# Kernel optimization log

Hardware: AMD Instinct MI355X
Metric: run time of the kernel (lower is better)

The kernel has to match this reference:

```python
import jax, jax.numpy as jnp
import numpy as np

# config (mirrors scaled-down DeepSeekModelConfig)
B, S, H = 2, 512, 1024          # batch, seq, hidden_size
E, I = 64, 512                  # n_routed_experts, moe_intermediate_size
K = 8                           # num_experts_per_tok
G, TG = 8, 4                    # n_group, topk_group
SCALE = 2.5                     # routed_scaling_factor
T = B * S                       # tokens
CAP = 512


def setup_inputs() -> dict:
    key = jax.random.key(0)
    ks = jax.random.split(key, 9)
    s_h = 1.0 / np.sqrt(H)
    s_i = 1.0 / np.sqrt(I)
    return {
        "x": jax.random.normal(ks[0], (B, S, H), jnp.float32),
        "router_w": jax.random.normal(ks[1], (H, E), jnp.float32) * s_h,
        "gate_w": jax.random.normal(ks[2], (E, H, I), jnp.float32) * s_h,
        "up_w": jax.random.normal(ks[3], (E, H, I), jnp.float32) * s_h,
        "down_w": jax.random.normal(ks[4], (E, I, H), jnp.float32) * s_i,
        "shared_gate_w": jax.random.normal(ks[5], (H, I), jnp.float32) * s_h,
        "shared_up_w": jax.random.normal(ks[6], (H, I), jnp.float32) * s_h,
        "shared_down_w": jax.random.normal(ks[7], (I, H), jnp.float32) * s_i,
    }


def _moe_forward(x, router_w, gate_w, up_w, down_w, shared_gate_w, shared_up_w, shared_down_w):
    b, s, h = x.shape
    tokens = x.reshape(-1, h)                              # [T, H]
    t = tokens.shape[0]

    # ---- router: sigmoid scores + grouped top-k masking ----
    logits = tokens @ router_w                             # [T, E]
    scores = jax.nn.sigmoid(logits)
    eg = E // G
    group_scores = scores.reshape(t, G, eg).max(axis=-1)   # [T, G]
    _, sel_groups = jax.lax.top_k(group_scores, TG)        # [T, TG]
    group_mask = jnp.zeros((t, G), bool).at[jnp.arange(t)[:, None], sel_groups].set(True)
    expert_mask = jnp.repeat(group_mask, eg, axis=1)       # [T, E]
    masked_scores = jnp.where(expert_mask, scores, 0.0)

    topk_w, topk_idx = jax.lax.top_k(masked_scores, K)     # [T, K]
    topk_w = topk_w / jnp.clip(topk_w.sum(-1, keepdims=True), 1e-9)
    topk_w = topk_w * SCALE

    # ---- dispatch: scatter tokens into per-expert capacity buffers ----
    flat_e = topk_idx.reshape(-1)                          # [T*K] expert id per assignment (row-major t,k)
    onehot = jax.nn.one_hot(flat_e, E, dtype=jnp.int32)    # [T*K, E]
    prior = jnp.cumsum(onehot, axis=0) - onehot            # exclusive count per expert
    pos = jnp.take_along_axis(prior, flat_e[:, None], axis=1)[:, 0]  # slot within expert
    valid = (pos < CAP).astype(tokens.dtype)               # [T*K]
    pos_c = jnp.minimum(pos, CAP - 1)
    tidx = jnp.repeat(jnp.arange(t), K)                    # token id per assignment

    dispatch = jnp.zeros((E, CAP, h), tokens.dtype)
    dispatch = dispatch.at[flat_e, pos_c].add(tokens[tidx] * valid[:, None])  # [E, C, H]

    # ---- per-expert SwiGLU (grouped GEMM) ----
    g = jnp.einsum('ech,ehi->eci', dispatch, gate_w)
    u = jnp.einsum('ech,ehi->eci', dispatch, up_w)
    expert_out = jnp.einsum('eci,eih->ech', jax.nn.silu(g) * u, down_w)       # [E, C, H]

    # ---- combine: gather back and weighted scatter-add ----
    gathered = expert_out[flat_e, pos_c]                   # [T*K, H]
    contrib = gathered * (topk_w.reshape(-1) * valid)[:, None]
    output = jnp.zeros((t, h), tokens.dtype).at[tidx].add(contrib)

    # ---- shared expert (n_shared_experts = 1) ----
    sg = jax.nn.silu(tokens @ shared_gate_w) * (tokens @ shared_up_w)
    output = output + sg @ shared_down_w
    return output.reshape(b, s, h)


def reference(x, router_w, gate_w, up_w, down_w, shared_gate_w, shared_up_w, shared_down_w):
    return _moe_forward(x, router_w, gate_w, up_w, down_w,
                        shared_gate_w, shared_up_w, shared_down_w)
```

## Files before the change

### kernel.cpp

```cpp
#include <hip/hip_runtime.h>
#include <hip/hip_bf16.h>

#define T_TOK 1024
#define H_DIM 1024
#define E_NUM 64
#define I_DIM 512
#define K_TOP 8
#define TG_NUM 4
#define CAPC 512
#define RSCALE 2.5f

typedef __attribute__((ext_vector_type(8))) short bf16x8;
typedef __attribute__((ext_vector_type(4))) float f32x4;

__device__ __forceinline__ ushort f2bf(float f) {
    union { float f; unsigned u; } v; v.f = f;
    unsigned r = v.u + 0x7fffu + ((v.u >> 16) & 1u);
    return (ushort)(r >> 16);
}
__device__ __forceinline__ unsigned pk2(float lo, float hi) {
    return (unsigned)f2bf(lo) | ((unsigned)f2bf(hi) << 16);
}
__device__ __forceinline__ void ldsbar() {
    asm volatile("s_waitcnt lgkmcnt(0)" ::: "memory");
    __builtin_amdgcn_s_barrier();
}

__global__ __launch_bounds__(256) void k_router(
    const float* __restrict__ x, const float* __restrict__ rw,
    ushort* __restrict__ xb,
    int* __restrict__ cnt, int* __restrict__ exp_tok,
    int* __restrict__ tslot, float* __restrict__ tw)
{
    const int t    = blockIdx.x;
    const int lane = threadIdx.x & 63;
    const int w    = threadIdx.x >> 6;

    {
        const float4 v = *(const float4*)&x[(size_t)t * H_DIM + threadIdx.x * 4];
        ushort4 o; o.x = f2bf(v.x); o.y = f2bf(v.y); o.z = f2bf(v.z); o.w = f2bf(v.w);
        *(ushort4*)&xb[(size_t)t * H_DIM + threadIdx.x * 4] = o;
    }

    const float* xp = x + (size_t)t * H_DIM + w * 256;
    const float* wp = rw + (size_t)(w * 256) * E_NUM + lane;
    float acc = 0.f;
    #pragma unroll 8
    for (int i = 0; i < 256; ++i)
        acc += xp[i] * wp[(size_t)i * E_NUM];

    __shared__ float part[4][64];
    part[w][lane] = acc;
    __syncthreads();
    if (threadIdx.x >= 64) return;

    float logit = part[0][lane] + part[1][lane] + part[2][lane] + part[3][lane];
    float score = 1.f / (1.f + expf(-logit));

    float gm = score;
    gm = fmaxf(gm, __shfl_xor(gm, 1));
    gm = fmaxf(gm, __shfl_xor(gm, 2));
    gm = fmaxf(gm, __shfl_xor(gm, 4));
    const int myg = lane >> 3;
    int grank = 0;
    #pragma unroll
    for (int j = 0; j < 8; ++j) {
        float gj = __shfl(gm, j * 8);
        grank += (gj > gm) || (gj == gm && j < myg);
    }
    float masked = (grank < TG_NUM) ? score : 0.f;

    int erank = 0;
    for (int j = 0; j < 64; ++j) {
        float sj = __shfl(masked, j);
        erank += (sj > masked) || (sj == masked && j < lane);
    }
    const bool keep = (erank < K_TOP);

    float kv = keep ? masked : 0.f;
    kv += __shfl_xor(kv, 1);  kv += __shfl_xor(kv, 2);  kv += __shfl_xor(kv, 4);
    kv += __shfl_xor(kv, 8);  kv += __shfl_xor(kv, 16); kv += __shfl_xor(kv, 32);
    const float wgt = masked / fmaxf(kv, 1e-9f) * RSCALE;

    if (keep) {
        int slot = atomicAdd(&cnt[lane], 1);
        if (slot < CAPC) {
            exp_tok[lane * CAPC + slot] = t;
            tslot[t * K_TOP + erank] = (lane << 9) | slot;
            tw[t * K_TOP + erank]    = wgt;
        } else {
            tslot[t * K_TOP + erank] = (lane << 9);
            tw[t * K_TOP + erank]    = 0.f;
        }
    }
}

__global__ void k_scan(const int* __restrict__ cnt, int* __restrict__ offs)
{
    const int lane = threadIdx.x;
    int v = min(cnt[lane], CAPC);
    #pragma unroll
    for (int off = 1; off < 64; off <<= 1) {
        int u = __shfl_up(v, off);
        if (lane >= off) v += u;
    }
    offs[lane + 1] = v;
    if (lane == 0) offs[0] = 0;
}

__global__ __launch_bounds__(512) void k_gemm1(
    const ushort* __restrict__ xb,
    const float* __restrict__ gate_w, const float* __restrict__ up_w,
    const float* __restrict__ sgate_w, const float* __restrict__ sup_w,
    const int* __restrict__ cnt, const int* __restrict__ offs,
    const int* __restrict__ exp_tok,
    ushort* __restrict__ hbuf)
{
    const int mt = blockIdx.x, nb = blockIdx.y, e = blockIdx.z;
    const bool sh = (e >= E_NUM);
    const int m0 = mt * 128;
    const int Me = sh ? 128 : min(cnt[e], CAPC);
    if (m0 >= Me) return;
    const int Mt = min(128, Me - m0);
    const int obase = sh ? (offs[E_NUM] + (e - E_NUM) * 128) : (offs[e] + m0);
    const float* gw = sh ? sgate_w : gate_w + (size_t)e * (H_DIM * I_DIM);
    const float* uw = sh ? sup_w  : up_w  + (size_t)e * (H_DIM * I_DIM);
    const int n0 = nb * 64;

    __shared__ ushort Bls[2 * 2 * 4096];

    const int tid  = threadIdx.x;
    const int lane = tid & 63, wid = tid >> 6;
    const int wm = wid >> 1, wn = wid & 1;
    const int fr = lane & 15, fg = lane >> 4;

    const int r0 = wm * 32 + fr, r1 = r0 + 16;
    int t0, t1;
    if (sh) { t0 = (e - E_NUM) * 128 + r0; t1 = (e - E_NUM) * 128 + r1; }
    else {
        t0 = (r0 < Mt) ? exp_tok[e * CAPC + m0 + r0] : 0;
        t1 = (r1 < Mt) ? exp_tok[e * CAPC + m0 + r1] : 0;
    }
    const ushort* a0p = xb + (size_t)t0 * H_DIM + fg * 8;
    const ushort* a1p = xb + (size_t)t1 * H_DIM + fg * 8;

    const int kp = tid >> 4, q = tid & 15;
    const float* gp = gw + (size_t)(2 * kp) * I_DIM + n0 + q * 4;
    const float* up = uw + (size_t)(2 * kp) * I_DIM + n0 + q * 4;
    const int wbe = (kp >> 2) * 512 + (kp & 3) * 2 + q * 32;

    f32x4 accg[2][2], accu[2][2];
    #pragma unroll
    for (int a = 0; a < 2; ++a)
        #pragma unroll
        for (int b = 0; b < 2; ++b) { accg[a][b] = (f32x4)0.f; accu[a][b] = (f32x4)0.f; }

    float4 pg0 = *(const float4*)gp;
    float4 pg1 = *(const float4*)(gp + I_DIM);
    float4 pu0 = *(const float4*)up;
    float4 pu1 = *(const float4*)(up + I_DIM);

    const int NT = H_DIM / 64;
    for (int kt = 0; kt < NT; ++kt) {
        float4 g0 = pg0, g1 = pg1, u0 = pu0, u1 = pu1;
        ushort* bw = &Bls[(kt & 1) * 8192 + wbe];
        #pragma unroll
        for (int j = 0; j < 4; ++j) {
            *(unsigned*)&bw[j * 8]        = pk2(((const float*)&g0)[j], ((const float*)&g1)[j]);
            *(unsigned*)&bw[4096 + j * 8] = pk2(((const float*)&u0)[j], ((const float*)&u1)[j]);
        }
        ldsbar();

        bf16x8 a00 = *(const bf16x8*)&a0p[kt * 64];
        bf16x8 a01 = *(const bf16x8*)&a0p[kt * 64 + 32];
        bf16x8 a10 = *(const bf16x8*)&a1p[kt * 64];
        bf16x8 a11 = *(const bf16x8*)&a1p[kt * 64 + 32];

        if (kt < NT - 1) {
            const float* gn = gp + (size_t)(kt + 1) * 64 * I_DIM;
            const float* un = up + (size_t)(kt + 1) * 64 * I_DIM;
            pg0 = *(const float4*)gn;  pg1 = *(const float4*)(gn + I_DIM);
            pu0 = *(const float4*)un;  pu1 = *(const float4*)(un + I_DIM);
        }

        const ushort* br = &Bls[(kt & 1) * 8192 + fg * 512 + (wn * 32 + fr) * 8];
        #pragma unroll
        for (int ks = 0; ks < 2; ++ks) {
            bf16x8 bg0 = *(const bf16x8*)&br[ks * 2048];
            bf16x8 bg1 = *(const bf16x8*)&br[ks * 2048 + 128];
            bf16x8 bu0 = *(const bf16x8*)&br[4096 + ks * 2048];
            bf16x8 bu1 = *(const bf16x8*)&br[4096 + ks * 2048 + 128];
            bf16x8 aa0 = ks ? a01 : a00;
            bf16x8 aa1 = ks ? a11 : a10;
            accg[0][0] = __builtin_amdgcn_mfma_f32_16x16x32_bf16(aa0, bg0, accg[0][0], 0, 0, 0);
            accg[0][1] = __builtin_amdgcn_mfma_f32_16x16x32_bf16(aa0, bg1, accg[0][1], 0, 0, 0);
            accg[1][0] = __builtin_amdgcn_mfma_f32_16x16x32_bf16(aa1, bg0, accg[1][0], 0, 0, 0);
            accg[1][1] = __builtin_amdgcn_mfma_f32_16x16x32_bf16(aa1, bg1, accg[1][1], 0, 0, 0);
            accu[0][0] = __builtin_amdgcn_mfma_f32_16x16x32_bf16(aa0, bu0, accu[0][0], 0, 0, 0);
            accu[0][1] = __builtin_amdgcn_mfma_f32_16x16x32_bf16(aa0, bu1, accu[0][1], 0, 0, 0);
            accu[1][0] = __builtin_amdgcn_mfma_f32_16x16x32_bf16(aa1, bu0, accu[1][0], 0, 0, 0);
            accu[1][1] = __builtin_amdgcn_mfma_f32_16x16x32_bf16(aa1, bu1, accu[1][1], 0, 0, 0);
        }
    }

    #pragma unroll
    for (int fm = 0; fm < 2; ++fm)
        #pragma unroll
        for (int fn = 0; fn < 2; ++fn)
            #pragma unroll
            for (int r = 0; r < 4; ++r) {
                const int l = wm * 32 + fm * 16 + fg * 4 + r;
                if (l < Mt) {
                    float g = accg[fm][fn][r];
                    float u = accu[fm][fn][r];
                    float h = g / (1.f + expf(-g)) * u;
                    hbuf[(size_t)(obase + l) * I_DIM + n0 + wn * 32 + fn * 16 + fr] = f2bf(h);
                }
            }
}

__global__ __launch_bounds__(512) void k_gemm2(
    const ushort* __restrict__ hbuf,
    const float* __restrict__ down_w, const float* __restrict__ sdown_w,
    const int* __restrict__ cnt, const int* __restrict__ offs,
    float* __restrict__ obuf)
{
    const int mt = blockIdx.x, nb = blockIdx.y, e = blockIdx.z;
    const bool sh = (e >= E_NUM);
    const int m0 = mt * 128;
    const int Me = sh ? 128 : min(cnt[e], CAPC);
    if (m0 >= Me) return;
    const int Mt = min(128, Me - m0);
    const int obase = sh ? (offs[E_NUM] + (e - E_NUM) * 128) : (offs[e] + m0);
    const float* dw = sh ? sdown_w : down_w + (size_t)e * (I_DIM * H_DIM);
    const int n0 = nb * 64;

    __shared__ ushort Bls[2 * 4096];

    const int tid  = threadIdx.x;
    const int lane = tid & 63, wid = tid >> 6;
    const int wm = wid >> 1, wn = wid & 1;
    const int fr = lane & 15, fg = lane >> 4;

    const ushort* a0p = hbuf + (size_t)(obase + wm * 32 + fr) * I_DIM + fg * 8;
    const ushort* a1p = a0p + (size_t)16 * I_DIM;

    const int kp = tid >> 4, q = tid & 15;
    const float* gp = dw + (size_t)(2 * kp) * H_DIM + n0 + q * 4;
    const int wbe = (kp >> 2) * 512 + (kp & 3) * 2 + q * 32;

    f32x4 acc[2][2];
    #pragma unroll
    for (int a = 0; a < 2; ++a)
        #pragma unroll
        for (int b = 0; b < 2; ++b) acc[a][b] = (f32x4)0.f;

    float4 pg0 = *(const float4*)gp;
    float4 pg1 = *(const float4*)(gp + H_DIM);

    const int NT = I_DIM / 64;
    for (int kt = 0; kt < NT; ++kt) {
        float4 g0 = pg0, g1 = pg1;
        ushort* bw = &Bls[(kt & 1) * 4096 + wbe];
        #pragma unroll
        for (int j = 0; j < 4; ++j)
            *(unsigned*)&bw[j * 8] = pk2(((const float*)&g0)[j], ((const float*)&g1)[j]);
        ldsbar();

        bf16x8 a00 = *(const bf16x8*)&a0p[kt * 64];
        bf16x8 a01 = *(const bf16x8*)&a0p[kt * 64 + 32];
        bf16x8 a10 = *(const bf16x8*)&a1p[kt * 64];
        bf16x8 a11 = *(const bf16x8*)&a1p[kt * 64 + 32];

        if (kt < NT - 1) {
            const float* gn = gp + (size_t)(kt + 1) * 64 * H_DIM;
            pg0 = *(const float4*)gn;  pg1 = *(const float4*)(gn + H_DIM);
        }

        const ushort* br = &Bls[(kt & 1) * 4096 + fg * 512 + (wn * 32 + fr) * 8];
        #pragma unroll
        for (int ks = 0; ks < 2; ++ks) {
            bf16x8 b0 = *(const bf16x8*)&br[ks * 2048];
            bf16x8 b1 = *(const bf16x8*)&br[ks * 2048 + 128];
            bf16x8 aa0 = ks ? a01 : a00;
            bf16x8 aa1 = ks ? a11 : a10;
            acc[0][0] = __builtin_amdgcn_mfma_f32_16x16x32_bf16(aa0, b0, acc[0][0], 0, 0, 0);
            acc[0][1] = __builtin_amdgcn_mfma_f32_16x16x32_bf16(aa0, b1, acc[0][1], 0, 0, 0);
            acc[1][0] = __builtin_amdgcn_mfma_f32_16x16x32_bf16(aa1, b0, acc[1][0], 0, 0, 0);
            acc[1][1] = __builtin_amdgcn_mfma_f32_16x16x32_bf16(aa1, b1, acc[1][1], 0, 0, 0);
        }
    }

    #pragma unroll
    for (int fm = 0; fm < 2; ++fm)
        #pragma unroll
        for (int fn = 0; fn < 2; ++fn)
            #pragma unroll
            for (int r = 0; r < 4; ++r) {
                const int l = wm * 32 + fm * 16 + fg * 4 + r;
                if (l < Mt)
                    obuf[(size_t)(obase + l) * H_DIM + n0 + wn * 32 + fn * 16 + fr] = acc[fm][fn][r];
            }
}

__global__ __launch_bounds__(256) void k_combine(
    const float* __restrict__ obuf, const int* __restrict__ offs,
    const int* __restrict__ tslot, const float* __restrict__ tw,
    float* __restrict__ out)
{
    const int t = blockIdx.x;
    __shared__ int   rs[8];
    __shared__ float wss[8];
    if (threadIdx.x < 8) {
        int id = tslot[t * K_TOP + threadIdx.x];
        rs[threadIdx.x]  = offs[id >> 9] + (id & 511);
        wss[threadIdx.x] = tw[t * K_TOP + threadIdx.x];
    }
    __syncthreads();
    const int c = threadIdx.x * 4;
    const int shrow = offs[E_NUM] + t;
    float4 acc = *(const float4*)&obuf[(size_t)shrow * H_DIM + c];
    #pragma unroll
    for (int j = 0; j < 8; ++j) {
        float4 v = *(const float4*)&obuf[(size_t)rs[j] * H_DIM + c];
        float w = wss[j];
        acc.x += w * v.x; acc.y += w * v.y; acc.z += w * v.z; acc.w += w * v.w;
    }
    *(float4*)&out[(size_t)t * H_DIM + c] = acc;
}

extern "C" void kernel_launch(void* const* d_in, const int* in_sizes, int n_in,
                              void* d_out, int out_size, void* d_ws, size_t ws_size,
                              hipStream_t stream)
{
    const float* x       = (const float*)d_in[0];
    const float* rw      = (const float*)d_in[1];
    const float* gate_w  = (const float*)d_in[2];
    const float* up_w    = (const float*)d_in[3];
    const float* down_w  = (const float*)d_in[4];
    const float* sgate_w = (const float*)d_in[5];
    const float* sup_w   = (const float*)d_in[6];
    const float* sdown_w = (const float*)d_in[7];
    float* out = (float*)d_out;

    char* ws = (char*)d_ws;
    int*    cnt     = (int*)(ws + 0);
    int*    offs    = (int*)(ws + 256);
    int*    exp_tok = (int*)(ws + 1024);
    int*    tslot   = (int*)(ws + 1024 + 131072);
    float*  tw      = (float*)(ws + 1024 + 131072 + 32768);
    ushort* xb      = (ushort*)(ws + (512u << 10));
    ushort* hbuf    = (ushort*)(ws + (3u << 20));
    float*  obuf    = (float*)(ws + (13u << 20));

    hipMemsetAsync(cnt, 0, 256, stream);
    k_router<<<T_TOK, 256, 0, stream>>>(x, rw, xb, cnt, exp_tok, tslot, tw);
    k_scan<<<1, 64, 0, stream>>>(cnt, offs);
    k_gemm1<<<dim3(2, 8, 72), 512, 0, stream>>>(xb, gate_w, up_w, sgate_w, sup_w,
                                                cnt, offs, exp_tok, hbuf);
    k_gemm2<<<dim3(2, 16, 72), 512, 0, stream>>>(hbuf, down_w, sdown_w, cnt, offs, obuf);
    k_combine<<<T_TOK, 256, 0, stream>>>(obuf, offs, tslot, tw, out);
}
```

Measured before the change: 542.7 us.

## Deepen weight/activation prefetch and use coalesced scalar weight loads in expert GEMMs

Both expert GEMM kernels now prefetch fp32 weights two K-tiles ahead and activation fragments one tile ahead in register double buffers, with the K loop fully unrolled. Weight loads change from per-thread float4 to strided scalar loads (q, q+16, ...), so adjacent lanes read adjacent addresses, and the LDS write pattern is remapped to match. Launch bounds now request 4 blocks per CU. The aim is to hide global-load latency behind MFMA work, at the cost of more registers and more load instructions, and the occupancy hint may force register spills.

```diff
diff --git a/kernel.cpp b/kernel.cpp
--- a/kernel.cpp
+++ b/kernel.cpp
@@ -108,7 +108,7 @@
     if (lane == 0) offs[0] = 0;
 }
 
-__global__ __launch_bounds__(512) void k_gemm1(
+__global__ __launch_bounds__(512, 4) void k_gemm1(
     const ushort* __restrict__ xb,
     const float* __restrict__ gate_w, const float* __restrict__ up_w,
     const float* __restrict__ sgate_w, const float* __restrict__ sup_w,
@@ -127,7 +127,7 @@
     const float* uw = sh ? sup_w  : up_w  + (size_t)e * (H_DIM * I_DIM);
     const int n0 = nb * 64;
 
-    __shared__ ushort Bls[2 * 2 * 4096];
+    __shared__ ushort Bls[2 * 8192];
 
     const int tid  = threadIdx.x;
     const int lane = tid & 63, wid = tid >> 6;
@@ -145,9 +145,10 @@
     const ushort* a1p = xb + (size_t)t1 * H_DIM + fg * 8;
 
     const int kp = tid >> 4, q = tid & 15;
-    const float* gp = gw + (size_t)(2 * kp) * I_DIM + n0 + q * 4;
-    const float* up = uw + (size_t)(2 * kp) * I_DIM + n0 + q * 4;
-    const int wbe = (kp >> 2) * 512 + (kp & 3) * 2 + q * 32;
+    const int kc = kp >> 2, c = kp & 3;
+    const float* gp  = gw + (size_t)(2 * kp) * I_DIM + n0 + q;
+    const float* upp = uw + (size_t)(2 * kp) * I_DIM + n0 + q;
+    const int wbase = kc * 512 + q * 8 + c * 2;
 
     f32x4 accg[2][2], accu[2][2];
     #pragma unroll
@@ -155,43 +156,46 @@
         #pragma unroll
         for (int b = 0; b < 2; ++b) { accg[a][b] = (f32x4)0.f; accu[a][b] = (f32x4)0.f; }
 
-    float4 pg0 = *(const float4*)gp;
-    float4 pg1 = *(const float4*)(gp + I_DIM);
-    float4 pu0 = *(const float4*)up;
-    float4 pu1 = *(const float4*)(up + I_DIM);
-
-    const int NT = H_DIM / 64;
-    for (int kt = 0; kt < NT; ++kt) {
-        float4 g0 = pg0, g1 = pg1, u0 = pu0, u1 = pu1;
-        ushort* bw = &Bls[(kt & 1) * 8192 + wbe];
+    float wg0[2][4], wg1[2][4], wu0[2][4], wu1[2][4];
+    bf16x8 av[2][4];
+
+#define LOADW1(p, kt) {                                                        \
+    const float* g_ = gp  + (size_t)(kt) * 64 * I_DIM;                         \
+    const float* u_ = upp + (size_t)(kt) * 64 * I_DIM;                         \
+    wg0[p][0]=g_[0];  wg0[p][1]=g_[16]; wg0[p][2]=g_[32]; wg0[p][3]=g_[48];    \
+    wg1[p][0]=g_[I_DIM]; wg1[p][1]=g_[I_DIM+16]; wg1[p][2]=g_[I_DIM+32]; wg1[p][3]=g_[I_DIM+48]; \
+    wu0[p][0]=u_[0];  wu0[p][1]=u_[16]; wu0[p][2]=u_[32]; wu0[p][3]=u_[48];    \
+    wu1[p][0]=u_[I_DIM]; wu1[p][1]=u_[I_DIM+16]; wu1[p][2]=u_[I_DIM+32]; wu1[p][3]=u_[I_DIM+48]; }
+#define LOADA1(p, kt) {                                                        \
+    av[p][0] = *(const bf16x8*)&a0p[(kt) * 64];                                \
+    av[p][1] = *(const bf16x8*)&a0p[(kt) * 64 + 32];                           \
+    av[p][2] = *(const bf16x8*)&a1p[(kt) * 64];                                \
+    av[p][3] = *(const bf16x8*)&a1p[(kt) * 64 + 32]; }
+
+    LOADW1(0, 0); LOADA1(0, 0); LOADW1(1, 1);
+
+    #pragma unroll
+    for (int kt = 0; kt < 16; ++kt) {
+        const int p = kt & 1;
+        ushort* bw = &Bls[p * 8192 + wbase];
         #pragma unroll
         for (int j = 0; j < 4; ++j) {
-            *(unsigned*)&bw[j * 8]        = pk2(((const float*)&g0)[j], ((const float*)&g1)[j]);
-            *(unsigned*)&bw[4096 + j * 8] = pk2(((const float*)&u0)[j], ((const float*)&u1)[j]);
+            *(unsigned*)&bw[j * 128]        = pk2(wg0[p][j], wg1[p][j]);
+            *(unsigned*)&bw[4096 + j * 128] = pk2(wu0[p][j], wu1[p][j]);
         }
         ldsbar();
-
-        bf16x8 a00 = *(const bf16x8*)&a0p[kt * 64];
-        bf16x8 a01 = *(const bf16x8*)&a0p[kt * 64 + 32];
-        bf16x8 a10 = *(const bf16x8*)&a1p[kt * 64];
-        bf16x8 a11 = *(const bf16x8*)&a1p[kt * 64 + 32];
-
-        if (kt < NT - 1) {
-            const float* gn = gp + (size_t)(kt + 1) * 64 * I_DIM;
-            const float* un = up + (size_t)(kt + 1) * 64 * I_DIM;
-            pg0 = *(const float4*)gn;  pg1 = *(const float4*)(gn + I_DIM);
-            pu0 = *(const float4*)un;  pu1 = *(const float4*)(un + I_DIM);
-        }
-
-        const ushort* br = &Bls[(kt & 1) * 8192 + fg * 512 + (wn * 32 + fr) * 8];
+        if (kt + 2 < 16) LOADW1(p, kt + 2);
+        if (kt + 1 < 16) LOADA1(1 - p, kt + 1);
+
+        const ushort* br = &Bls[p * 8192 + fg * 512 + (wn * 32 + fr) * 8];
         #pragma unroll
         for (int ks = 0; ks < 2; ++ks) {
             bf16x8 bg0 = *(const bf16x8*)&br[ks * 2048];
             bf16x8 bg1 = *(const bf16x8*)&br[ks * 2048 + 128];
             bf16x8 bu0 = *(const bf16x8*)&br[4096 + ks * 2048];
             bf16x8 bu1 = *(const bf16x8*)&br[4096 + ks * 2048 + 128];
-            bf16x8 aa0 = ks ? a01 : a00;
-            bf16x8 aa1 = ks ? a11 : a10;
+            bf16x8 aa0 = ks ? av[p][1] : av[p][0];
+            bf16x8 aa1 = ks ? av[p][3] : av[p][2];
             accg[0][0] = __builtin_amdgcn_mfma_f32_16x16x32_bf16(aa0, bg0, accg[0][0], 0, 0, 0);
             accg[0][1] = __builtin_amdgcn_mfma_f32_16x16x32_bf16(aa0, bg1, accg[0][1], 0, 0, 0);
             accg[1][0] = __builtin_amdgcn_mfma_f32_16x16x32_bf16(aa1, bg0, accg[1][0], 0, 0, 0);
@@ -202,6 +206,8 @@
             accu[1][1] = __builtin_amdgcn_mfma_f32_16x16x32_bf16(aa1, bu1, accu[1][1], 0, 0, 0);
         }
     }
+#undef LOADW1
+#undef LOADA1
 
     #pragma unroll
     for (int fm = 0; fm < 2; ++fm)
@@ -219,7 +225,7 @@
             }
 }
 
-__global__ __launch_bounds__(512) void k_gemm2(
+__global__ __launch_bounds__(512, 4) void k_gemm2(
     const ushort* __restrict__ hbuf,
     const float* __restrict__ down_w, const float* __restrict__ sdown_w,
     const int* __restrict__ cnt, const int* __restrict__ offs,
@@ -246,8 +252,9 @@
     const ushort* a1p = a0p + (size_t)16 * I_DIM;
 
     const int kp = tid >> 4, q = tid & 15;
-    const float* gp = dw + (size_t)(2 * kp) * H_DIM + n0 + q * 4;
-    const int wbe = (kp >> 2) * 512 + (kp & 3) * 2 + q * 32;
+    const int kc = kp >> 2, c = kp & 3;
+    const float* dp = dw + (size_t)(2 * kp) * H_DIM + n0 + q;
+    const int wbase = kc * 512 + q * 8 + c * 2;
 
     f32x4 acc[2][2];
     #pragma unroll
@@ -255,41 +262,47 @@
         #pragma unroll
         for (int b = 0; b < 2; ++b) acc[a][b] = (f32x4)0.f;
 
-    float4 pg0 = *(const float4*)gp;
-    float4 pg1 = *(const float4*)(gp + H_DIM);
-
-    const int NT = I_DIM / 64;
-    for (int kt = 0; kt < NT; ++kt) {
-        float4 g0 = pg0, g1 = pg1;
-        ushort* bw = &Bls[(kt & 1) * 4096 + wbe];
+    float wd0[2][4], wd1[2][4];
+    bf16x8 av[2][4];
+
+#define LOADW2(p, kt) {                                                        \
+    const float* d_ = dp + (size_t)(kt) * 64 * H_DIM;                          \
+    wd0[p][0]=d_[0];  wd0[p][1]=d_[16]; wd0[p][2]=d_[32]; wd0[p][3]=d_[48];    \
+    wd1[p][0]=d_[H_DIM]; wd1[p][1]=d_[H_DIM+16]; wd1[p][2]=d_[H_DIM+32]; wd1[p][3]=d_[H_DIM+48]; }
+#define LOADA2(p, kt) {                                                        \
+    av[p][0] = *(const bf16x8*)&a0p[(kt) * 64];                                \
+    av[p][1] = *(const bf16x8*)&a0p[(kt) * 64 + 32];                           \
+    av[p][2] = *(const bf16x8*)&a1p[(kt) * 64];                                \
+    av[p][3] = *(const bf16x8*)&a1p[(kt) * 64 + 32]; }
+
+    LOADW2(0, 0); LOADA2(0, 0); LOADW2(1, 1);
+
+    #pragma unroll
+    for (int kt = 0; kt < 8; ++kt) {
+        const int p = kt & 1;
+        ushort* bw = &Bls[p * 4096 + wbase];
         #pragma unroll
         for (int j = 0; j < 4; ++j)
-            *(unsigned*)&bw[j * 8] = pk2(((const float*)&g0)[j], ((const float*)&g1)[j]);
+            *(unsigned*)&bw[j * 128] = pk2(wd0[p][j], wd1[p][j]);
         ldsbar();
-
-        bf16x8 a00 = *(const bf16x8*)&a0p[kt * 64];
-        bf16x8 a01 = *(const bf16x8*)&a0p[kt * 64 + 32];
-        bf16x8 a10 = *(const bf16x8*)&a1p[kt * 64];
-        bf16x8 a11 = *(const bf16x8*)&a1p[kt * 64 + 32];
-
-        if (kt < NT - 1) {
-            const float* gn = gp + (size_t)(kt + 1) * 64 * H_DIM;
-            pg0 = *(const float4*)gn;  pg1 = *(const float4*)(gn + H_DIM);
-        }
-
-        const ushort* br = &Bls[(kt & 1) * 4096 + fg * 512 + (wn * 32 + fr) * 8];
+        if (kt + 2 < 8) LOADW2(p, kt + 2);
+        if (kt + 1 < 8) LOADA2(1 - p, kt + 1);
+
+        const ushort* br = &Bls[p * 4096 + fg * 512 + (wn * 32 + fr) * 8];
         #pragma unroll
         for (int ks = 0; ks < 2; ++ks) {
             bf16x8 b0 = *(const bf16x8*)&br[ks * 2048];
             bf16x8 b1 = *(const bf16x8*)&br[ks * 2048 + 128];
-            bf16x8 aa0 = ks ? a01 : a00;
-            bf16x8 aa1 = ks ? a11 : a10;
+            bf16x8 aa0 = ks ? av[p][1] : av[p][0];
+            bf16x8 aa1 = ks ? av[p][3] : av[p][2];
             acc[0][0] = __builtin_amdgcn_mfma_f32_16x16x32_bf16(aa0, b0, acc[0][0], 0, 0, 0);
             acc[0][1] = __builtin_amdgcn_mfma_f32_16x16x32_bf16(aa0, b1, acc[0][1], 0, 0, 0);
             acc[1][0] = __builtin_amdgcn_mfma_f32_16x16x32_bf16(aa1, b0, acc[1][0], 0, 0, 0);
             acc[1][1] = __builtin_amdgcn_mfma_f32_16x16x32_bf16(aa1, b1, acc[1][1], 0, 0, 0);
         }
     }
+#undef LOADW2
+#undef LOADA2
 
     #pragma unroll
     for (int fm = 0; fm < 2; ++fm)
```

Measured after the change: 541.5 us. About the same (-0.2%).

## Loop over M tiles per block and deepen weight prefetch pipeline in expert GEMMs

Applied to the files above, without the earlier changes.

Each block in both grouped GEMMs now walks every 128-row M tile of its expert instead of launching a separate block per M tile. The grid drops a dimension and blocks whose tile would be empty are no longer launched. The K loop is restructured into an even/odd double-buffered pipeline with a K-step of 32, a smaller LDS footprint, float2 weight loads, and a launch-bounds occupancy hint of 4. Blocks handling experts with more than 128 tokens re-read and re-convert the fp32 weights for each tile. Heavily loaded experts are also serialised within one block, which may hurt load balance.

```diff
diff --git a/kernel.cpp b/kernel.cpp
--- a/kernel.cpp
+++ b/kernel.cpp
@@ -12,6 +12,8 @@
 
 typedef __attribute__((ext_vector_type(8))) short bf16x8;
 typedef __attribute__((ext_vector_type(4))) float f32x4;
+
+#define MFMA_BF16 __builtin_amdgcn_mfma_f32_16x16x32_bf16
 
 __device__ __forceinline__ ushort f2bf(float f) {
     union { float f; unsigned u; } v; v.f = f;
@@ -108,7 +110,7 @@
     if (lane == 0) offs[0] = 0;
 }
 
-__global__ __launch_bounds__(512) void k_gemm1(
+__global__ __launch_bounds__(512, 4) void k_gemm1(
     const ushort* __restrict__ xb,
     const float* __restrict__ gate_w, const float* __restrict__ up_w,
     const float* __restrict__ sgate_w, const float* __restrict__ sup_w,
@@ -116,191 +118,184 @@
     const int* __restrict__ exp_tok,
     ushort* __restrict__ hbuf)
 {
-    const int mt = blockIdx.x, nb = blockIdx.y, e = blockIdx.z;
+    const int nb = blockIdx.x, e = blockIdx.y;
     const bool sh = (e >= E_NUM);
-    const int m0 = mt * 128;
     const int Me = sh ? 128 : min(cnt[e], CAPC);
-    if (m0 >= Me) return;
-    const int Mt = min(128, Me - m0);
-    const int obase = sh ? (offs[E_NUM] + (e - E_NUM) * 128) : (offs[e] + m0);
+    const int ebase = sh ? (offs[E_NUM] + (e - E_NUM) * 128) : offs[e];
     const float* gw = sh ? sgate_w : gate_w + (size_t)e * (H_DIM * I_DIM);
     const float* uw = sh ? sup_w  : up_w  + (size_t)e * (H_DIM * I_DIM);
     const int n0 = nb * 64;
 
-    __shared__ ushort Bls[2 * 2 * 4096];
+    __shared__ ushort Bls[2 * 4096];
 
     const int tid  = threadIdx.x;
     const int lane = tid & 63, wid = tid >> 6;
     const int wm = wid >> 1, wn = wid & 1;
     const int fr = lane & 15, fg = lane >> 4;
 
-    const int r0 = wm * 32 + fr, r1 = r0 + 16;
-    int t0, t1;
-    if (sh) { t0 = (e - E_NUM) * 128 + r0; t1 = (e - E_NUM) * 128 + r1; }
-    else {
-        t0 = (r0 < Mt) ? exp_tok[e * CAPC + m0 + r0] : 0;
-        t1 = (r1 < Mt) ? exp_tok[e * CAPC + m0 + r1] : 0;
-    }
-    const ushort* a0p = xb + (size_t)t0 * H_DIM + fg * 8;
-    const ushort* a1p = xb + (size_t)t1 * H_DIM + fg * 8;
-
-    const int kp = tid >> 4, q = tid & 15;
-    const float* gp = gw + (size_t)(2 * kp) * I_DIM + n0 + q * 4;
-    const float* up = uw + (size_t)(2 * kp) * I_DIM + n0 + q * 4;
-    const int wbe = (kp >> 2) * 512 + (kp & 3) * 2 + q * 32;
-
-    f32x4 accg[2][2], accu[2][2];
-    #pragma unroll
-    for (int a = 0; a < 2; ++a)
-        #pragma unroll
-        for (int b = 0; b < 2; ++b) { accg[a][b] = (f32x4)0.f; accu[a][b] = (f32x4)0.f; }
-
-    float4 pg0 = *(const float4*)gp;
-    float4 pg1 = *(const float4*)(gp + I_DIM);
-    float4 pu0 = *(const float4*)up;
-    float4 pu1 = *(const float4*)(up + I_DIM);
-
-    const int NT = H_DIM / 64;
-    for (int kt = 0; kt < NT; ++kt) {
-        float4 g0 = pg0, g1 = pg1, u0 = pu0, u1 = pu1;
-        ushort* bw = &Bls[(kt & 1) * 8192 + wbe];
-        #pragma unroll
-        for (int j = 0; j < 4; ++j) {
-            *(unsigned*)&bw[j * 8]        = pk2(((const float*)&g0)[j], ((const float*)&g1)[j]);
-            *(unsigned*)&bw[4096 + j * 8] = pk2(((const float*)&u0)[j], ((const float*)&u1)[j]);
+    const int kp = tid >> 5, q = tid & 31;
+    const int kc = kp >> 2, c = kp & 3;
+    const float* gp  = gw + (size_t)(2 * kp) * I_DIM + n0 + 2 * q;
+    const float* upp = uw + (size_t)(2 * kp) * I_DIM + n0 + 2 * q;
+    const int wb = kc * 512 + q * 16 + c * 2;
+
+#define LW1(S, kt) { const float* g_ = gp  + (size_t)(kt) * 32 * I_DIM;        \
+                     const float* u_ = upp + (size_t)(kt) * 32 * I_DIM;        \
+                     ga##S = *(const float2*)g_;  gb##S = *(const float2*)(g_ + I_DIM); \
+                     ua##S = *(const float2*)u_;  ub##S = *(const float2*)(u_ + I_DIM); }
+#define LA1(S, kt) { a0##S = *(const bf16x8*)&a0p[(kt) * 32];                  \
+                     a1##S = *(const bf16x8*)&a1p[(kt) * 32]; }
+#define SW1(S, bo) { ushort* bw = &Bls[(bo) + wb];                             \
+                     *(unsigned*)&bw[0]        = pk2(ga##S.x, gb##S.x);        \
+                     *(unsigned*)&bw[8]        = pk2(ga##S.y, gb##S.y);        \
+                     *(unsigned*)&bw[2048]     = pk2(ua##S.x, ub##S.x);        \
+                     *(unsigned*)&bw[2048 + 8] = pk2(ua##S.y, ub##S.y); }
+#define MM1(A0, A1, bo) {                                                      \
+    const ushort* br = &Bls[(bo) + fg * 512 + (wn * 32 + fr) * 8];             \
+    bf16x8 bg0 = *(const bf16x8*)&br[0];                                       \
+    bf16x8 bg1 = *(const bf16x8*)&br[128];                                     \
+    bf16x8 bu0 = *(const bf16x8*)&br[2048];                                    \
+    bf16x8 bu1 = *(const bf16x8*)&br[2176];                                    \
+    accg00 = MFMA_BF16(A0, bg0, accg00, 0, 0, 0);                              \
+    accg01 = MFMA_BF16(A0, bg1, accg01, 0, 0, 0);                              \
+    accg10 = MFMA_BF16(A1, bg0, accg10, 0, 0, 0);                              \
+    accg11 = MFMA_BF16(A1, bg1, accg11, 0, 0, 0);                              \
+    accu00 = MFMA_BF16(A0, bu0, accu00, 0, 0, 0);                              \
+    accu01 = MFMA_BF16(A0, bu1, accu01, 0, 0, 0);                              \
+    accu10 = MFMA_BF16(A1, bu0, accu10, 0, 0, 0);                              \
+    accu11 = MFMA_BF16(A1, bu1, accu11, 0, 0, 0); }
+
+    for (int m0 = 0; m0 < Me; m0 += 128) {
+        const int Mt = min(128, Me - m0);
+        const int obase = ebase + m0;
+        const int r0 = wm * 32 + fr, r1 = r0 + 16;
+        int t0, t1;
+        if (sh) { t0 = (e - E_NUM) * 128 + r0; t1 = t0 + 16; }
+        else {
+            t0 = (r0 < Mt) ? exp_tok[e * CAPC + m0 + r0] : 0;
+            t1 = (r1 < Mt) ? exp_tok[e * CAPC + m0 + r1] : 0;
         }
-        ldsbar();
-
-        bf16x8 a00 = *(const bf16x8*)&a0p[kt * 64];
-        bf16x8 a01 = *(const bf16x8*)&a0p[kt * 64 + 32];
-        bf16x8 a10 = *(const bf16x8*)&a1p[kt * 64];
-        bf16x8 a11 = *(const bf16x8*)&a1p[kt * 64 + 32];
-
-        if (kt < NT - 1) {
-            const float* gn = gp + (size_t)(kt + 1) * 64 * I_DIM;
-            const float* un = up + (size_t)(kt + 1) * 64 * I_DIM;
-            pg0 = *(const float4*)gn;  pg1 = *(const float4*)(gn + I_DIM);
-            pu0 = *(const float4*)un;  pu1 = *(const float4*)(un + I_DIM);
+        const ushort* a0p = xb + (size_t)t0 * H_DIM + fg * 8;
+        const ushort* a1p = xb + (size_t)t1 * H_DIM + fg * 8;
+
+        f32x4 accg00 = (f32x4)0.f, accg01 = (f32x4)0.f, accg10 = (f32x4)0.f, accg11 = (f32x4)0.f;
+        f32x4 accu00 = (f32x4)0.f, accu01 = (f32x4)0.f, accu10 = (f32x4)0.f, accu11 = (f32x4)0.f;
+        float2 gaE, gbE, uaE, ubE, gaO, gbO, uaO, ubO;
+        bf16x8 a0E, a1E, a0O, a1O;
+
+        LW1(E, 0); LA1(E, 0); LW1(O, 1);
+
+        for (int it = 0; it < 16; ++it) {
+            const int kt = it * 2;
+            SW1(E, 0);
+            ldsbar();
+            if (it < 15) LW1(E, kt + 2);
+            LA1(O, kt + 1);
+            MM1(a0E, a1E, 0);
+            SW1(O, 4096);
+            ldsbar();
+            if (it < 15) { LW1(O, kt + 3); LA1(E, kt + 2); }
+            MM1(a0O, a1O, 4096);
         }
 
-        const ushort* br = &Bls[(kt & 1) * 8192 + fg * 512 + (wn * 32 + fr) * 8];
-        #pragma unroll
-        for (int ks = 0; ks < 2; ++ks) {
-            bf16x8 bg0 = *(const bf16x8*)&br[ks * 2048];
-            bf16x8 bg1 = *(const bf16x8*)&br[ks * 2048 + 128];
-            bf16x8 bu0 = *(const bf16x8*)&br[4096 + ks * 2048];
-            bf16x8 bu1 = *(const bf16x8*)&br[4096 + ks * 2048 + 128];
-            bf16x8 aa0 = ks ? a01 : a00;
-            bf16x8 aa1 = ks ? a11 : a10;
-            accg[0][0] = __builtin_amdgcn_mfma_f32_16x16x32_bf16(aa0, bg0, accg[0][0], 0, 0, 0);
-            accg[0][1] = __builtin_amdgcn_mfma_f32_16x16x32_bf16(aa0, bg1, accg[0][1], 0, 0, 0);
-            accg[1][0] = __builtin_amdgcn_mfma_f32_16x16x32_bf16(aa1, bg0, accg[1][0], 0, 0, 0);
-            accg[1][1] = __builtin_amdgcn_mfma_f32_16x16x32_bf16(aa1, bg1, accg[1][1], 0, 0, 0);
-            accu[0][0] = __builtin_amdgcn_mfma_f32_16x16x32_bf16(aa0, bu0, accu[0][0], 0, 0, 0);
-            accu[0][1] = __builtin_amdgcn_mfma_f32_16x16x32_bf16(aa0, bu1, accu[0][1], 0, 0, 0);
-            accu[1][0] = __builtin_amdgcn_mfma_f32_16x16x32_bf16(aa1, bu0, accu[1][0], 0, 0, 0);
-            accu[1][1] = __builtin_amdgcn_mfma_f32_16x16x32_bf16(aa1, bu1, accu[1][1], 0, 0, 0);
-        }
-    }
-
-    #pragma unroll
-    for (int fm = 0; fm < 2; ++fm)
-        #pragma unroll
-        for (int fn = 0; fn < 2; ++fn)
-            #pragma unroll
-            for (int r = 0; r < 4; ++r) {
-                const int l = wm * 32 + fm * 16 + fg * 4 + r;
-                if (l < Mt) {
-                    float g = accg[fm][fn][r];
-                    float u = accu[fm][fn][r];
-                    float h = g / (1.f + expf(-g)) * u;
-                    hbuf[(size_t)(obase + l) * I_DIM + n0 + wn * 32 + fn * 16 + fr] = f2bf(h);
-                }
-            }
-}
-
-__global__ __launch_bounds__(512) void k_gemm2(
+#define EPI1(AG, AU, rowofs, colofs)                                           \
+        _Pragma("unroll")                                                      \
+        for (int r = 0; r < 4; ++r) {                                          \
+            const int l = wm * 32 + (rowofs) + fg * 4 + r;                     \
+            if (l < Mt) {                                                      \
+                const float g = AG[r], u = AU[r];                              \
+                const float h = g / (1.f + __expf(-g)) * u;                    \
+                hbuf[(size_t)(obase + l) * I_DIM + n0 + wn * 32 + (colofs) + fr] = f2bf(h); } }
+        EPI1(accg00, accu00, 0, 0);  EPI1(accg01, accu01, 0, 16);
+        EPI1(accg10, accu10, 16, 0); EPI1(accg11, accu11, 16, 16);
+#undef EPI1
+    }
+#undef LW1
+#undef LA1
+#undef SW1
+#undef MM1
+}
+
+__global__ __launch_bounds__(512, 4) void k_gemm2(
     const ushort* __restrict__ hbuf,
     const float* __restrict__ down_w, const float* __restrict__ sdown_w,
     const int* __restrict__ cnt, const int* __restrict__ offs,
     float* __restrict__ obuf)
 {
-    const int mt = blockIdx.x, nb = blockIdx.y, e = blockIdx.z;
+    const int nb = blockIdx.x, e = blockIdx.y;
     const bool sh = (e >= E_NUM);
-    const int m0 = mt * 128;
     const int Me = sh ? 128 : min(cnt[e], CAPC);
-    if (m0 >= Me) return;
-    const int Mt = min(128, Me - m0);
-    const int obase = sh ? (offs[E_NUM] + (e - E_NUM) * 128) : (offs[e] + m0);
+    const int ebase = sh ? (offs[E_NUM] + (e - E_NUM) * 128) : offs[e];
     const float* dw = sh ? sdown_w : down_w + (size_t)e * (I_DIM * H_DIM);
     const int n0 = nb * 64;
 
-    __shared__ ushort Bls[2 * 4096];
+    __shared__ ushort Bls[2 * 2048];
 
     const int tid  = threadIdx.x;
     const int lane = tid & 63, wid = tid >> 6;
     const int wm = wid >> 1, wn = wid & 1;
     const int fr = lane & 15, fg = lane >> 4;
 
-    const ushort* a0p = hbuf + (size_t)(obase + wm * 32 + fr) * I_DIM + fg * 8;
-    const ushort* a1p = a0p + (size_t)16 * I_DIM;
-
-    const int kp = tid >> 4, q = tid & 15;
-    const float* gp = dw + (size_t)(2 * kp) * H_DIM + n0 + q * 4;
-    const int wbe = (kp >> 2) * 512 + (kp & 3) * 2 + q * 32;
-
-    f32x4 acc[2][2];
-    #pragma unroll
-    for (int a = 0; a < 2; ++a)
-        #pragma unroll
-        for (int b = 0; b < 2; ++b) acc[a][b] = (f32x4)0.f;
-
-    float4 pg0 = *(const float4*)gp;
-    float4 pg1 = *(const float4*)(gp + H_DIM);
-
-    const int NT = I_DIM / 64;
-    for (int kt = 0; kt < NT; ++kt) {
-        float4 g0 = pg0, g1 = pg1;
-        ushort* bw = &Bls[(kt & 1) * 4096 + wbe];
-        #pragma unroll
-        for (int j = 0; j < 4; ++j)
-            *(unsigned*)&bw[j * 8] = pk2(((const float*)&g0)[j], ((const float*)&g1)[j]);
-        ldsbar();
-
-        bf16x8 a00 = *(const bf16x8*)&a0p[kt * 64];
-        bf16x8 a01 = *(const bf16x8*)&a0p[kt * 64 + 32];
-        bf16x8 a10 = *(const bf16x8*)&a1p[kt * 64];
-        bf16x8 a11 = *(const bf16x8*)&a1p[kt * 64 + 32];
-
-        if (kt < NT - 1) {
-            const float* gn = gp + (size_t)(kt + 1) * 64 * H_DIM;
-            pg0 = *(const float4*)gn;  pg1 = *(const float4*)(gn + H_DIM);
+    const int kp = tid >> 5, q = tid & 31;
+    const int kc = kp >> 2, c = kp & 3;
+    const float* dp = dw + (size_t)(2 * kp) * H_DIM + n0 + 2 * q;
+    const int wb = kc * 512 + q * 16 + c * 2;
+
+#define LW2(S, kt) { const float* d_ = dp + (size_t)(kt) * 32 * H_DIM;         \
+                     da##S = *(const float2*)d_;  db##S = *(const float2*)(d_ + H_DIM); }
+#define LA2(S, kt) { a0##S = *(const bf16x8*)&a0p[(kt) * 32];                  \
+                     a1##S = *(const bf16x8*)&a1p[(kt) * 32]; }
+#define SW2(S, bo) { ushort* bw = &Bls[(bo) + wb];                             \
+                     *(unsigned*)&bw[0] = pk2(da##S.x, db##S.x);               \
+                     *(unsigned*)&bw[8] = pk2(da##S.y, db##S.y); }
+#define MM2(A0, A1, bo) {                                                      \
+    const ushort* br = &Bls[(bo) + fg * 512 + (wn * 32 + fr) * 8];             \
+    bf16x8 b0 = *(const bf16x8*)&br[0];                                        \
+    bf16x8 b1 = *(const bf16x8*)&br[128];                                      \
+    ac00 = MFMA_BF16(A0, b0, ac00, 0, 0, 0);                                   \
+    ac01 = MFMA_BF16(A0, b1, ac01, 0, 0, 0);                                   \
+    ac10 = MFMA_BF16(A1, b0, ac10, 0, 0, 0);                                   \
+    ac11 = MFMA_BF16(A1, b1, ac11, 0, 0, 0); }
+
+    for (int m0 = 0; m0 < Me; m0 += 128) {
+        const int Mt = min(128, Me - m0);
+        const int obase = ebase + m0;
+        const ushort* a0p = hbuf + (size_t)(obase + wm * 32 + fr) * I_DIM + fg * 8;
+        const ushort* a1p = a0p + (size_t)16 * I_DIM;
+
+        f32x4 ac00 = (f32x4)0.f, ac01 = (f32x4)0.f, ac10 = (f32x4)0.f, ac11 = (f32x4)0.f;
+        float2 daE, dbE, daO, dbO;
+        bf16x8 a0E, a1E, a0O, a1O;
+
+        LW2(E, 0); LA2(E, 0); LW2(O, 1);
+
+        for (int it = 0; it < 8; ++it) {
+            const int kt = it * 2;
+            SW2(E, 0);
+            ldsbar();
+            if (it < 7) LW2(E, kt + 2);
+            LA2(O, kt + 1);
+            MM2(a0E, a1E, 0);
+            SW2(O, 2048);
+            ldsbar();
+            if (it < 7) { LW2(O, kt + 3); LA2(E, kt + 2); }
+            MM2(a0O, a1O, 2048);
         }
 
-        const ushort* br = &Bls[(kt & 1) * 4096 + fg * 512 + (wn * 32 + fr) * 8];
-        #pragma unroll
-        for (int ks = 0; ks < 2; ++ks) {
-            bf16x8 b0 = *(const bf16x8*)&br[ks * 2048];
-            bf16x8 b1 = *(const bf16x8*)&br[ks * 2048 + 128];
-            bf16x8 aa0 = ks ? a01 : a00;
-            bf16x8 aa1 = ks ? a11 : a10;
-            acc[0][0] = __builtin_amdgcn_mfma_f32_16x16x32_bf16(aa0, b0, acc[0][0], 0, 0, 0);
-            acc[0][1] = __builtin_amdgcn_mfma_f32_16x16x32_bf16(aa0, b1, acc[0][1], 0, 0, 0);
-            acc[1][0] = __builtin_amdgcn_mfma_f32_16x16x32_bf16(aa1, b0, acc[1][0], 0, 0, 0);
-            acc[1][1] = __builtin_amdgcn_mfma_f32_16x16x32_bf16(aa1, b1, acc[1][1], 0, 0, 0);
-        }
-    }
-
-    #pragma unroll
-    for (int fm = 0; fm < 2; ++fm)
-        #pragma unroll
-        for (int fn = 0; fn < 2; ++fn)
-            #pragma unroll
-            for (int r = 0; r < 4; ++r) {
-                const int l = wm * 32 + fm * 16 + fg * 4 + r;
-                if (l < Mt)
-                    obuf[(size_t)(obase + l) * H_DIM + n0 + wn * 32 + fn * 16 + fr] = acc[fm][fn][r];
-            }
+#define EPO2(AC, rowofs, colofs)                                               \
+        _Pragma("unroll")                                                      \
+        for (int r = 0; r < 4; ++r) {                                          \
+            const int l = wm * 32 + (rowofs) + fg * 4 + r;                     \
+            if (l < Mt)                                                        \
+                obuf[(size_t)(obase + l) * H_DIM + n0 + wn * 32 + (colofs) + fr] = AC[r]; }
+        EPO2(ac00, 0, 0);  EPO2(ac01, 0, 16);
+        EPO2(ac10, 16, 0); EPO2(ac11, 16, 16);
+#undef EPO2
+    }
+#undef LW2
+#undef LA2
+#undef SW2
+#undef MM2
 }
 
 __global__ __launch_bounds__(256) void k_combine(
@@ -356,8 +351,8 @@
     hipMemsetAsync(cnt, 0, 256, stream);
     k_router<<<T_TOK, 256, 0, stream>>>(x, rw, xb, cnt, exp_tok, tslot, tw);
     k_scan<<<1, 64, 0, stream>>>(cnt, offs);
-    k_gemm1<<<dim3(2, 8, 72), 512, 0, stream>>>(xb, gate_w, up_w, sgate_w, sup_w,
-                                                cnt, offs, exp_tok, hbuf);
-    k_gemm2<<<dim3(2, 16, 72), 512, 0, stream>>>(hbuf, down_w, sdown_w, cnt, offs, obuf);
+    k_gemm1<<<dim3(8, 72), 512, 0, stream>>>(xb, gate_w, up_w, sgate_w, sup_w,
+                                             cnt, offs, exp_tok, hbuf);
+    k_gemm2<<<dim3(16, 72), 512, 0, stream>>>(hbuf, down_w, sdown_w, cnt, offs, obuf);
     k_combine<<<T_TOK, 256, 0, stream>>>(obuf, offs, tslot, tw, out);
 }
```

Result: faster. 513.1 us (-5.5%).
